# Kernel tuning notes

Measured on AMD Instinct MI355X. Metric: run time of the kernel, lower is better.

The kernel has to match this reference:

```python
import jax, jax.numpy as jnp
import numpy as np

D = 1024      # n_embd
F = 1024      # moe_inter_dim (ffn_hidden_size)
E = 8         # moe_num_experts
K = 2         # moe_top_k
B, T = 2, 2048


def setup_inputs() -> dict:
    key = jax.random.key(0)
    ks = jax.random.split(key, 7)
    std = 0.02
    x = jax.random.normal(ks[0], (B, T, D), dtype=jnp.float32)
    router_w = jax.random.normal(ks[1], (D, E), dtype=jnp.float32) * std
    w1 = jax.random.normal(ks[2], (E, D, F), dtype=jnp.float32) * std  # expert up proj
    w2 = jax.random.normal(ks[3], (E, F, D), dtype=jnp.float32) * std  # expert down proj
    shared_gate_up = jax.random.normal(ks[4], (D, 2 * F), dtype=jnp.float32) * std
    shared_down = jax.random.normal(ks[5], (F, D), dtype=jnp.float32) * std
    shared_gate_w = jax.random.normal(ks[6], (D, 1), dtype=jnp.float32) * std
    return {"x": x, "router_w": router_w, "w1": w1, "w2": w2,
            "shared_gate_up": shared_gate_up, "shared_down": shared_down,
            "shared_gate_w": shared_gate_w}


def _moe_forward(x, router_w, w1, w2, shared_gate_up, shared_down, shared_gate_w):
    b, t, d = x.shape
    xf = x.reshape(-1, d)                                   # [N, D]
    n = xf.shape[0]

    # --- router: softmax over experts, top-k scores used directly as combine weights ---
    logits = xf @ router_w                                  # [N, E]
    probs = jax.nn.softmax(logits, axis=-1)
    topw, topi = jax.lax.top_k(probs, K)                    # [N, K]
    combine = jnp.zeros((n, E), dtype=probs.dtype).at[
        jnp.arange(n)[:, None], topi].add(topw)             # [N, E] sparse combine weights

    # --- expert MLP: h = silu(x @ w1_e) @ w2_e, combined with routing weights ---
    h = jax.nn.silu(jnp.einsum('nd,edf->nef', xf, w1))      # [N, E, F]
    ye = jnp.einsum('nef,efd->ned', h, w2)                  # [N, E, D]
    routed = jnp.einsum('ne,ned->nd', combine, ye)          # [N, D]

    # --- shared expert SwiGLU, gated by sigmoid(x @ shared_gate_w) ---
    gu = xf @ shared_gate_up                                # [N, 2F]
    gate, up = gu[:, :F], gu[:, F:]
    shared = (jax.nn.silu(gate) * up) @ shared_down         # [N, D]
    shared = jax.nn.sigmoid(xf @ shared_gate_w) * shared

    return (routed + shared).reshape(b, t, d)


def reference(x, router_w, w1, w2, shared_gate_up, shared_down, shared_gate_w):
    return _moe_forward(x, router_w, w1, w2, shared_gate_up, shared_down, shared_gate_w)
```

## Files before the change

kernel.cpp:

```cpp
#include <hip/hip_runtime.h>
#include <math.h>

typedef __bf16 bf16_t;
typedef __bf16 bf16x8 __attribute__((ext_vector_type(8)));
typedef __bf16 bf16x4 __attribute__((ext_vector_type(4)));
typedef float f32x4 __attribute__((ext_vector_type(4)));

#define N_TOK 4096
#define DMODEL 1024
#define FFN 1024
#define NEXP 8
#define HIST_BLK 16

#define BM 128
#define BN 128
#define BK 32

typedef __attribute__((address_space(3))) uint32_t lds_u32_t;
typedef const __attribute__((address_space(1))) uint32_t glb_u32_t;

__global__ void transpose_all_kernel(const float* __restrict__ w1, const float* __restrict__ w2,
                                     const float* __restrict__ sgu, const float* __restrict__ sdw,
                                     bf16_t* __restrict__ w1t, bf16_t* __restrict__ w2t,
                                     bf16_t* __restrict__ sgut, bf16_t* __restrict__ sdt) {
  __shared__ float tile[32][33];
  const int z = blockIdx.z;
  const float* in;
  bf16_t* out;
  int C = 1024;
  bool remap = false;
  if (z < 8) {
    in = w1 + (size_t)z * 1048576; out = w1t + (size_t)z * 1048576;
  } else if (z < 16) {
    in = w2 + (size_t)(z - 8) * 1048576; out = w2t + (size_t)(z - 8) * 1048576;
  } else if (z == 16) {
    in = sgu; out = sgut; C = 2048; remap = true;
  } else {
    in = sdw; out = sdt;
  }
  const int R = 1024;
  const int c0 = blockIdx.x * 32, r0 = blockIdx.y * 32;
  if (c0 >= C) return;
  const int tx = threadIdx.x, ty = threadIdx.y;
#pragma unroll
  for (int i = 0; i < 32; i += 8)
    tile[ty + i][tx] = in[(size_t)(r0 + ty + i) * C + (c0 + tx)];
  __syncthreads();
#pragma unroll
  for (int i = 0; i < 32; i += 8) {
    int c = c0 + ty + i;
    int oc = remap ? ((c < FFN) ? 2 * c : 2 * (c - FFN) + 1) : c;
    out[(size_t)oc * R + (r0 + tx)] = (bf16_t)tile[tx][ty + i];
  }
}

__global__ void router_kernel(const float* __restrict__ x, const float* __restrict__ rw,
                              const float* __restrict__ gw, bf16_t* __restrict__ xb,
                              int* __restrict__ topi, float* __restrict__ topw,
                              float* __restrict__ sig) {
  const int t = blockIdx.x;
  const int lane = threadIdx.x;
  const float* xr = x + (size_t)t * DMODEL;
  bf16_t* xbr = xb + (size_t)t * DMODEL;
  float acc[NEXP] = {0.f, 0.f, 0.f, 0.f, 0.f, 0.f, 0.f, 0.f};
  float accg = 0.f;
#pragma unroll
  for (int i = 0; i < 4; i++) {
    const int d = i * 256 + lane * 4;
    float4 xv = *reinterpret_cast<const float4*>(xr + d);
    bf16x4 o;
    o[0] = (bf16_t)xv.x; o[1] = (bf16_t)xv.y; o[2] = (bf16_t)xv.z; o[3] = (bf16_t)xv.w;
    *reinterpret_cast<bf16x4*>(xbr + d) = o;
    const float xs[4] = {xv.x, xv.y, xv.z, xv.w};
#pragma unroll
    for (int j = 0; j < 4; j++) {
      const float4* r = reinterpret_cast<const float4*>(rw + (size_t)(d + j) * NEXP);
      float4 r0 = r[0], r1 = r[1];
      float xj = xs[j];
      acc[0] += xj * r0.x; acc[1] += xj * r0.y; acc[2] += xj * r0.z; acc[3] += xj * r0.w;
      acc[4] += xj * r1.x; acc[5] += xj * r1.y; acc[6] += xj * r1.z; acc[7] += xj * r1.w;
      accg += xj * gw[d + j];
    }
  }
#pragma unroll
  for (int e = 0; e < NEXP; e++)
    for (int s = 32; s > 0; s >>= 1) acc[e] += __shfl_down(acc[e], s, 64);
  for (int s = 32; s > 0; s >>= 1) accg += __shfl_down(accg, s, 64);
  if (lane == 0) {
    float mx = acc[0];
#pragma unroll
    for (int e = 1; e < NEXP; e++) mx = fmaxf(mx, acc[e]);
    float p[NEXP], sum = 0.f;
#pragma unroll
    for (int e = 0; e < NEXP; e++) { p[e] = __expf(acc[e] - mx); sum += p[e]; }
    int i1 = 0;
#pragma unroll
    for (int e = 1; e < NEXP; e++) if (acc[e] > acc[i1]) i1 = e;
    int i2 = (i1 == 0) ? 1 : 0;
#pragma unroll
    for (int e = 0; e < NEXP; e++) if (e != i1 && acc[e] > acc[i2]) i2 = e;
    float inv = 1.f / sum;
    topi[2 * t] = i1;     topw[2 * t] = p[i1] * inv;
    topi[2 * t + 1] = i2; topw[2 * t + 1] = p[i2] * inv;
    sig[t] = 1.f / (1.f + __expf(-accg));
  }
}

__global__ void hist_kernel(const int* __restrict__ topi, int* __restrict__ block_counts) {
  __shared__ int h[NEXP];
  const int tid = threadIdx.x;
  if (tid < NEXP) h[tid] = 0;
  __syncthreads();
  const int t = blockIdx.x * 256 + tid;
  atomicAdd(&h[topi[2 * t]], 1);
  atomicAdd(&h[topi[2 * t + 1]], 1);
  __syncthreads();
  if (tid < NEXP) block_counts[blockIdx.x * NEXP + tid] = h[tid];
}

__global__ void scan_kernel(const int* __restrict__ block_counts, int* __restrict__ offsets,
                            int* __restrict__ counts, int* __restrict__ block_base) {
  int o = 0;
  for (int e = 0; e < NEXP; e++) {
    int tot = 0;
    for (int b = 0; b < HIST_BLK; b++) {
      block_base[b * NEXP + e] = o + tot;
      tot += block_counts[b * NEXP + e];
    }
    offsets[e] = o;
    counts[e] = tot;
    o += tot;
  }
}

__global__ void gather_kernel(const int* __restrict__ topi, const float* __restrict__ topw,
                              const int* __restrict__ block_base, int* __restrict__ slot_tok,
                              float* __restrict__ slot_w, int* __restrict__ slot_of) {
  __shared__ int cur[NEXP];
  const int tid = threadIdx.x;
  if (tid < NEXP) cur[tid] = block_base[blockIdx.x * NEXP + tid];
  __syncthreads();
  const int t = blockIdx.x * 256 + tid;
#pragma unroll
  for (int j = 0; j < 2; j++) {
    int e = topi[2 * t + j];
    int s = atomicAdd(&cur[e], 1);
    slot_tok[s] = t;
    slot_w[s] = topw[2 * t + j];
    slot_of[2 * t + j] = s;
  }
}

__global__ void combine_kernel(const bf16_t* __restrict__ Y, const int* __restrict__ slot_of,
                               float* __restrict__ out) {
  int i = blockIdx.x * blockDim.x + threadIdx.x;
  int t = i >> 7;
  int d = (i & 127) << 3;
  int s0 = slot_of[2 * t], s1 = slot_of[2 * t + 1];
  bf16x8 a = *reinterpret_cast<const bf16x8*>(Y + (size_t)s0 * DMODEL + d);
  bf16x8 b = *reinterpret_cast<const bf16x8*>(Y + (size_t)s1 * DMODEL + d);
  float* o = out + (size_t)t * DMODEL + d;
  float4 o0 = *reinterpret_cast<float4*>(o);
  float4 o1 = *reinterpret_cast<float4*>(o + 4);
  o0.x += (float)a[0] + (float)b[0]; o0.y += (float)a[1] + (float)b[1];
  o0.z += (float)a[2] + (float)b[2]; o0.w += (float)a[3] + (float)b[3];
  o1.x += (float)a[4] + (float)b[4]; o1.y += (float)a[5] + (float)b[5];
  o1.z += (float)a[6] + (float)b[6]; o1.w += (float)a[7] + (float)b[7];
  *reinterpret_cast<float4*>(o) = o0;
  *reinterpret_cast<float4*>(o + 4) = o1;
}

template <int PHASE>
__global__ __launch_bounds__(256) void moe_gemm_kernel(
    const bf16_t* __restrict__ A0, const bf16_t* __restrict__ B0,
    const bf16_t* __restrict__ A1, const bf16_t* __restrict__ B1,
    void* __restrict__ C0, void* __restrict__ C1,
    const int* __restrict__ offsets, const int* __restrict__ counts,
    const int* __restrict__ slot_tok, const float* __restrict__ slot_w,
    const float* __restrict__ sig) {
  __shared__ bf16_t lds_a[BM * BK];
  __shared__ bf16_t lds_b[BN * BK];

  const int z = blockIdx.z;
  int m0, mEnd;
  const bf16_t *Ap, *Bp;
  if (z == 0) {
    m0 = blockIdx.y * BM;
    mEnd = N_TOK;
    Ap = A0; Bp = B0;
  } else {
    if (PHASE == 0 && blockIdx.x >= FFN / BN) return;
    const int e = z - 1;
    m0 = offsets[e] + (int)blockIdx.y * BM;
    mEnd = offsets[e] + counts[e];
    if (m0 >= mEnd) return;
    Ap = A1; Bp = B1 + (size_t)e * FFN * DMODEL;
  }
  const int n0 = blockIdx.x * BN;

  const int tid = threadIdx.x;
  const int lane = tid & 63;
  const int wave = tid >> 6;
  const int qd = lane >> 4;
  const int lm = lane & 15;
  const int wm = (wave >> 1) * 64;
  const int wn = (wave & 1) * 64;

  const int cc = lane & 3;
  const int rr = lane >> 2;
  const bf16_t* pa[2];
  const bf16_t* pb[2];
#pragma unroll
  for (int i = 0; i < 2; i++) {
    int r = wave * 32 + i * 16 + rr;
    int s = m0 + r;
    int g;
    if (z == 0) g = s;
    else if (PHASE == 0) g = slot_tok[(s < mEnd) ? s : (mEnd - 1)];
    else g = (s < mEnd) ? s : (mEnd - 1);
    pa[i] = Ap + (size_t)g * 1024 + cc * 8;
    pb[i] = Bp + (size_t)(n0 + r) * 1024 + cc * 8;
  }

  f32x4 acc[4][4] = {};

  for (int k0 = 0; k0 < 1024; k0 += BK) {
    __syncthreads();
#pragma unroll
    for (int i = 0; i < 2; i++) {
      __builtin_amdgcn_global_load_lds((glb_u32_t*)(pa[i] + k0),
                                       (lds_u32_t*)&lds_a[(wave * 32 + i * 16) * BK], 16, 0, 0);
      __builtin_amdgcn_global_load_lds((glb_u32_t*)(pb[i] + k0),
                                       (lds_u32_t*)&lds_b[(wave * 32 + i * 16) * BK], 16, 0, 0);
    }
    __syncthreads();
    bf16x8 af[4], bfr[4];
#pragma unroll
    for (int i = 0; i < 4; i++)
      af[i] = *reinterpret_cast<const bf16x8*>(&lds_a[(wm + i * 16 + lm) * BK + qd * 8]);
#pragma unroll
    for (int j = 0; j < 4; j++)
      bfr[j] = *reinterpret_cast<const bf16x8*>(&lds_b[(wn + j * 16 + lm) * BK + qd * 8]);
#pragma unroll
    for (int i = 0; i < 4; i++)
#pragma unroll
      for (int j = 0; j < 4; j++)
        acc[i][j] = __builtin_amdgcn_mfma_f32_16x16x32_bf16(af[i], bfr[j], acc[i][j], 0, 0, 0);
  }

#pragma unroll
  for (int i = 0; i < 4; i++) {
#pragma unroll
    for (int r = 0; r < 4; r++) {
      const int gm = m0 + wm + i * 16 + qd * 4 + r;
      const bool mOk = (z == 0) || (gm < mEnd);
#pragma unroll
      for (int j = 0; j < 4; j++) {
        const int col = n0 + wn + j * 16 + lm;
        float v = acc[i][j][r];
        if (PHASE == 0) {
          if (z == 0) {
            float u = __shfl_xor(v, 1, 64);
            if ((lane & 1) == 0) {
              float sv = v / (1.f + __expf(-v)) * u;
              ((bf16_t*)C0)[(size_t)gm * FFN + (col >> 1)] = (bf16_t)sv;
            }
          } else if (mOk) {
            ((bf16_t*)C1)[(size_t)gm * FFN + col] = (bf16_t)(v / (1.f + __expf(-v)));
          }
        } else {
          if (z == 0) {
            ((float*)C0)[(size_t)gm * DMODEL + col] = sig[gm] * v;
          } else if (mOk) {
            ((bf16_t*)C1)[(size_t)gm * DMODEL + col] = (bf16_t)(slot_w[gm] * v);
          }
        }
      }
    }
  }
}

extern "C" void kernel_launch(void* const* d_in, const int* in_sizes, int n_in, void* d_out,
                              int out_size, void* d_ws, size_t ws_size, hipStream_t stream) {
  const float* x = (const float*)d_in[0];
  const float* rw = (const float*)d_in[1];
  const float* w1 = (const float*)d_in[2];
  const float* w2 = (const float*)d_in[3];
  const float* sgu = (const float*)d_in[4];
  const float* sdw = (const float*)d_in[5];
  const float* gw = (const float*)d_in[6];
  float* out = (float*)d_out;

  char* ws = (char*)d_ws;
  size_t off = 0;
  auto alloc = [&](size_t bytes) -> void* {
    void* p = ws + off;
    off += (bytes + 255) & ~(size_t)255;
    return p;
  };
  bf16_t* xb = (bf16_t*)alloc((size_t)N_TOK * DMODEL * 2);
  bf16_t* w1t = (bf16_t*)alloc((size_t)NEXP * DMODEL * FFN * 2);
  bf16_t* w2t = (bf16_t*)alloc((size_t)NEXP * DMODEL * FFN * 2);
  bf16_t* sgut = (bf16_t*)alloc((size_t)2 * FFN * DMODEL * 2);
  bf16_t* sdt = (bf16_t*)alloc((size_t)DMODEL * FFN * 2);
  bf16_t* S = (bf16_t*)alloc((size_t)N_TOK * FFN * 2);
  bf16_t* H = (bf16_t*)alloc((size_t)N_TOK * 2 * FFN * 2);
  bf16_t* Y = (bf16_t*)alloc((size_t)N_TOK * 2 * DMODEL * 2);
  int* topi = (int*)alloc(N_TOK * 2 * 4);
  float* topw = (float*)alloc(N_TOK * 2 * 4);
  float* sig = (float*)alloc(N_TOK * 4);
  int* slot_tok = (int*)alloc(N_TOK * 2 * 4);
  float* slot_w = (float*)alloc(N_TOK * 2 * 4);
  int* slot_of = (int*)alloc(N_TOK * 2 * 4);
  int* block_counts = (int*)alloc(HIST_BLK * NEXP * 4);
  int* block_base = (int*)alloc(HIST_BLK * NEXP * 4);
  int* counts = (int*)alloc(NEXP * 4);
  int* offsets = (int*)alloc(NEXP * 4);

  transpose_all_kernel<<<dim3(64, 32, 18), dim3(32, 8), 0, stream>>>(w1, w2, sgu, sdw, w1t, w2t,
                                                                     sgut, sdt);
  router_kernel<<<N_TOK, 64, 0, stream>>>(x, rw, gw, xb, topi, topw, sig);
  hist_kernel<<<HIST_BLK, 256, 0, stream>>>(topi, block_counts);
  scan_kernel<<<1, 1, 0, stream>>>(block_counts, offsets, counts, block_base);
  gather_kernel<<<HIST_BLK, 256, 0, stream>>>(topi, topw, block_base, slot_tok, slot_w, slot_of);

  moe_gemm_kernel<0><<<dim3(2 * FFN / BN, N_TOK / BM, 1 + NEXP), 256, 0, stream>>>(
      xb, sgut, xb, w1t, S, H, offsets, counts, slot_tok, slot_w, sig);
  moe_gemm_kernel<1><<<dim3(DMODEL / BN, N_TOK / BM, 1 + NEXP), 256, 0, stream>>>(
      S, sdt, H, w2t, out, Y, offsets, counts, slot_tok, slot_w, sig);
  combine_kernel<<<N_TOK * DMODEL / 8 / 256, 256, 0, stream>>>(Y, slot_of, out);
}
```

Before: 326.1 us.

## Register-prefetch GEMM tiles and pad LDS rows to avoid bank conflicts

Replaces direct global-to-LDS loads with register-staged loads: the next K tile is fetched into registers while MFMAs run on the current LDS tile, then written to LDS at the next iteration. LDS rows are padded from 32 to 40 bf16 elements so the 16-byte fragment reads spread across banks. This costs extra VGPRs and LDS traffic through registers, and it issues a wasted wraparound load on the last iteration.

```diff
diff --git a/kernel.cpp b/kernel.cpp
--- a/kernel.cpp
+++ b/kernel.cpp
@@ -15,9 +15,7 @@
 #define BM 128
 #define BN 128
 #define BK 32
-
-typedef __attribute__((address_space(3))) uint32_t lds_u32_t;
-typedef const __attribute__((address_space(1))) uint32_t glb_u32_t;
+#define LDK 40
 
 __global__ void transpose_all_kernel(const float* __restrict__ w1, const float* __restrict__ w2,
                                      const float* __restrict__ sgu, const float* __restrict__ sdw,
@@ -178,8 +176,8 @@
     const int* __restrict__ offsets, const int* __restrict__ counts,
     const int* __restrict__ slot_tok, const float* __restrict__ slot_w,
     const float* __restrict__ sig) {
-  __shared__ bf16_t lds_a[BM * BK];
-  __shared__ bf16_t lds_b[BN * BK];
+  __shared__ bf16_t lds_a[BM * LDK];
+  __shared__ bf16_t lds_b[BN * LDK];
 
   const int z = blockIdx.z;
   int m0, mEnd;
@@ -206,20 +204,26 @@
   const int wm = (wave >> 1) * 64;
   const int wn = (wave & 1) * 64;
 
-  const int cc = lane & 3;
-  const int rr = lane >> 2;
+  const int arow = tid >> 2;
+  const int cc = tid & 3;
   const bf16_t* pa[2];
   const bf16_t* pb[2];
 #pragma unroll
-  for (int i = 0; i < 2; i++) {
-    int r = wave * 32 + i * 16 + rr;
-    int s = m0 + r;
+  for (int h = 0; h < 2; h++) {
+    int s = m0 + arow + h * 64;
     int g;
     if (z == 0) g = s;
     else if (PHASE == 0) g = slot_tok[(s < mEnd) ? s : (mEnd - 1)];
     else g = (s < mEnd) ? s : (mEnd - 1);
-    pa[i] = Ap + (size_t)g * 1024 + cc * 8;
-    pb[i] = Bp + (size_t)(n0 + r) * 1024 + cc * 8;
+    pa[h] = Ap + (size_t)g * 1024 + cc * 8;
+    pb[h] = Bp + (size_t)(n0 + arow + h * 64) * 1024 + cc * 8;
+  }
+
+  uint4 ra[2], rb[2];
+#pragma unroll
+  for (int h = 0; h < 2; h++) {
+    ra[h] = *reinterpret_cast<const uint4*>(pa[h]);
+    rb[h] = *reinterpret_cast<const uint4*>(pb[h]);
   }
 
   f32x4 acc[4][4] = {};
@@ -227,20 +231,24 @@
   for (int k0 = 0; k0 < 1024; k0 += BK) {
     __syncthreads();
 #pragma unroll
-    for (int i = 0; i < 2; i++) {
-      __builtin_amdgcn_global_load_lds((glb_u32_t*)(pa[i] + k0),
-                                       (lds_u32_t*)&lds_a[(wave * 32 + i * 16) * BK], 16, 0, 0);
-      __builtin_amdgcn_global_load_lds((glb_u32_t*)(pb[i] + k0),
-                                       (lds_u32_t*)&lds_b[(wave * 32 + i * 16) * BK], 16, 0, 0);
+    for (int h = 0; h < 2; h++) {
+      *reinterpret_cast<uint4*>(&lds_a[(arow + h * 64) * LDK + cc * 8]) = ra[h];
+      *reinterpret_cast<uint4*>(&lds_b[(arow + h * 64) * LDK + cc * 8]) = rb[h];
     }
     __syncthreads();
+    const int kn = (k0 + BK) & 1023;
+#pragma unroll
+    for (int h = 0; h < 2; h++) {
+      ra[h] = *reinterpret_cast<const uint4*>(pa[h] + kn);
+      rb[h] = *reinterpret_cast<const uint4*>(pb[h] + kn);
+    }
     bf16x8 af[4], bfr[4];
 #pragma unroll
     for (int i = 0; i < 4; i++)
-      af[i] = *reinterpret_cast<const bf16x8*>(&lds_a[(wm + i * 16 + lm) * BK + qd * 8]);
+      af[i] = *reinterpret_cast<const bf16x8*>(&lds_a[(wm + i * 16 + lm) * LDK + qd * 8]);
 #pragma unroll
     for (int j = 0; j < 4; j++)
-      bfr[j] = *reinterpret_cast<const bf16x8*>(&lds_b[(wn + j * 16 + lm) * BK + qd * 8]);
+      bfr[j] = *reinterpret_cast<const bf16x8*>(&lds_b[(wn + j * 16 + lm) * LDK + qd * 8]);
 #pragma unroll
     for (int i = 0; i < 4; i++)
 #pragma unroll
```

Result: slower. 631.2 us (+93.6%).
